# Performance work log

Measured on AMD Instinct MI355X. Metric: run time of the kernel, lower is better.

The kernel has to match this reference:

```python
import jax, jax.numpy as jnp
import numpy as np

B, S = 8, 2048
CHANNELS, DIM, HEADS = 256, 3, 6
TCH = CHANNELS * 2  # 512
EPS = 1e-5


def _linear_init(key, out_f, in_f):
    # torch nn.Linear default init: U(-1/sqrt(in_f), 1/sqrt(in_f)) for W and b
    k1, k2 = jax.random.split(key)
    bound = 1.0 / np.sqrt(in_f)
    w = jax.random.uniform(k1, (out_f, in_f), jnp.float32, -bound, bound)
    b = jax.random.uniform(k2, (out_f,), jnp.float32, -bound, bound)
    return w, b


def setup_inputs() -> dict:
    key = jax.random.key(0)
    ks = jax.random.split(key, 8)
    x = jax.random.normal(ks[0], (B, S, TCH), jnp.float32)
    wq, bq = _linear_init(ks[1], DIM, TCH)
    wk, bk = _linear_init(ks[2], DIM, TCH)
    wv, bv = _linear_init(ks[3], DIM, TCH)
    wo, bo = _linear_init(ks[4], TCH, HEADS * DIM)
    w1, b1 = _linear_init(ks[5], TCH, TCH)
    w2, b2 = _linear_init(ks[6], TCH, TCH)
    gamma = jnp.ones((TCH,), jnp.float32)
    beta = jnp.zeros((TCH,), jnp.float32)
    return {"x": x, "wq": wq, "bq": bq, "wk": wk, "bk": bk, "wv": wv, "bv": bv,
            "wo": wo, "bo": bo, "w1": w1, "b1": b1, "w2": w2, "b2": b2,
            "gamma": gamma, "beta": beta}


def _layernorm(x, gamma, beta):
    mu = jnp.mean(x, axis=-1, keepdims=True)
    var = jnp.mean(jnp.square(x - mu), axis=-1, keepdims=True)
    return (x - mu) * jax.lax.rsqrt(var + EPS) * gamma + beta


def reference(x, wq, bq, wk, bk, wv, bv, wo, bo, w1, b1, w2, b2, gamma, beta):
    # All heads share the same w_q/w_k/w_v, so one attention pass suffices;
    # concatenating HEADS copies reproduces the original math exactly.
    q = x @ wq.T + bq                      # [B,S,DIM]
    k = x @ wk.T + bk                      # [B,S,DIM]
    v = x @ wv.T + bv                      # [B,S,DIM]
    scores = jnp.einsum('bqd,bkd->bqk', q, k) / np.sqrt(DIM)  # [B,S,S]
    soft = jax.nn.softmax(scores, axis=-1)
    z = jnp.einsum('bqk,bkd->bqd', soft, v)  # [B,S,DIM]
    z = jnp.concatenate([z] * HEADS, axis=-1)  # [B,S,HEADS*DIM]
    z = z @ wo.T + bo                       # [B,S,TCH]
    r0 = x + (z @ w1.T + b1)
    r1 = _layernorm(r0, gamma, beta)
    r1 = r1 @ w2.T + b2
    r = r0 + r1
    return _layernorm(r, gamma, beta)
```

## Files before the change

kernel.cpp:

```cpp
#include <hip/hip_runtime.h>
#include <hip/hip_bf16.h>

#define TCH 512
#define MTOT 16384
#define SEQ 2048
#define LN_EPS 1e-5f

typedef __attribute__((ext_vector_type(8))) __bf16 bf16x8;
typedef __attribute__((ext_vector_type(4))) float f32x4;

__device__ __forceinline__ unsigned pkbf(float a, float b) {
  union { __hip_bfloat16 h; unsigned short u; } ca, cb;
  ca.h = __float2bfloat16(a); cb.h = __float2bfloat16(b);
  return (unsigned)ca.u | ((unsigned)cb.u << 16);
}
__device__ __forceinline__ float bf_lo(unsigned u) { return __uint_as_float(u << 16); }
__device__ __forceinline__ float bf_hi(unsigned u) { return __uint_as_float(u & 0xffff0000u); }

__device__ __forceinline__ bf16x8 cvt8(float4 a, float4 b) {
  union { __hip_bfloat16 h; __bf16 v; } u;
  bf16x8 r;
  u.h = __float2bfloat16(a.x); r[0] = u.v;
  u.h = __float2bfloat16(a.y); r[1] = u.v;
  u.h = __float2bfloat16(a.z); r[2] = u.v;
  u.h = __float2bfloat16(a.w); r[3] = u.v;
  u.h = __float2bfloat16(b.x); r[4] = u.v;
  u.h = __float2bfloat16(b.y); r[5] = u.v;
  u.h = __float2bfloat16(b.z); r[6] = u.v;
  u.h = __float2bfloat16(b.w); r[7] = u.v;
  return r;
}

#define QSCALE 0.8329517853860118f

__global__ __launch_bounds__(256) void prep_kernel(
    const float* __restrict__ w1, const float* __restrict__ w2,
    const float* __restrict__ wo, const float* __restrict__ bo,
    const float* __restrict__ wq, const float* __restrict__ bq,
    const float* __restrict__ wk, const float* __restrict__ bk,
    const float* __restrict__ wv, const float* __restrict__ bv,
    __hip_bfloat16* __restrict__ w1b, __hip_bfloat16* __restrict__ w2b,
    float4* __restrict__ wo_eff4,
    __hip_bfloat16* __restrict__ wqkvb, float* __restrict__ qkvbias)
{
  int i = blockIdx.x * 256 + threadIdx.x;
  w1b[i] = __float2bfloat16(w1[i]);
  w2b[i] = __float2bfloat16(w2[i]);
  if (i < TCH) {
    float s0 = 0.f, s1 = 0.f, s2 = 0.f;
    #pragma unroll
    for (int h = 0; h < 6; ++h) {
      s0 += wo[i*18 + h*3 + 0];
      s1 += wo[i*18 + h*3 + 1];
      s2 += wo[i*18 + h*3 + 2];
    }
    wo_eff4[i] = make_float4(s0, s1, s2, bo[i]);
  }
  if (i < 16 * TCH) {
    int row = i >> 9, k = i & 511;
    float v;
    if      (row < 3) v = wq[row * TCH + k] * QSCALE;
    else if (row < 6) v = wk[(row - 3) * TCH + k];
    else if (row < 9) v = wv[(row - 6) * TCH + k];
    else              v = 0.f;
    wqkvb[i] = __float2bfloat16(v);
  }
  if (i < 16) {
    float v;
    if      (i < 3) v = bq[i] * QSCALE;
    else if (i < 6) v = bk[i - 3];
    else if (i < 9) v = bv[i - 6];
    else            v = 0.f;
    qkvbias[i] = v;
  }
}

__global__ __launch_bounds__(256) void qkv_kernel(
    const float* __restrict__ x,
    const __hip_bfloat16* __restrict__ wqkvb, const float* __restrict__ qkvbias,
    float4* __restrict__ q4, uint4* __restrict__ kvp,
    __hip_bfloat16* __restrict__ xb)
{
  const int t = threadIdx.x, wv = t >> 6, ln = t & 63;
  const int l16 = ln & 15, quad = ln >> 4;
  const int row0 = blockIdx.x * 64 + wv * 16;

  bf16x8 bfr[16];
  #pragma unroll
  for (int ks = 0; ks < 16; ++ks)
    bfr[ks] = *reinterpret_cast<const bf16x8*>(wqkvb + l16 * TCH + ks * 32 + quad * 8);

  const float* xp = x + (size_t)(row0 + l16) * TCH + quad * 8;
  __hip_bfloat16* xo = xb + (size_t)(row0 + l16) * TCH + quad * 8;

  float4 xa0 = *(const float4*)xp,        xb0 = *(const float4*)(xp + 4);
  float4 xa1 = *(const float4*)(xp + 32), xb1 = *(const float4*)(xp + 36);
  f32x4 acc = {};
  #pragma unroll
  for (int ks = 0; ks < 16; ++ks) {
    float4 xa2 = {}, xb2 = {};
    if (ks < 14) {
      xa2 = *(const float4*)(xp + (ks + 2) * 32);
      xb2 = *(const float4*)(xp + (ks + 2) * 32 + 4);
    }
    bf16x8 af = cvt8(xa0, xb0);
    *reinterpret_cast<bf16x8*>(xo + ks * 32) = af;
    acc = __builtin_amdgcn_mfma_f32_16x16x32_bf16(af, bfr[ks], acc, 0, 0, 0);
    xa0 = xa1; xb0 = xb1; xa1 = xa2; xb1 = xb2;
  }

  __shared__ float tr[4][16][17];
  #pragma unroll
  for (int r = 0; r < 4; ++r) tr[wv][quad * 4 + r][l16] = acc[r];
  __syncthreads();

  if (ln < 32) {
    const int row  = ln & 15;
    const int grow = row0 + row;
    float c[9];
    #pragma unroll
    for (int j = 0; j < 9; ++j) c[j] = tr[wv][row][j] + qkvbias[j];
    if (ln < 16) {
      q4[grow] = make_float4(c[0], c[1], c[2], 0.f);
    } else {
      kvp[grow] = make_uint4(pkbf(c[3], c[4]), pkbf(c[5], c[6]), pkbf(c[7], c[8]), 0u);
    }
  }
}

__global__ __launch_bounds__(1024) void attn_kernel(
    const float4* __restrict__ q4, const uint4* __restrict__ kvp,
    const float4* __restrict__ wo_eff4,
    __hip_bfloat16* __restrict__ z2b)
{
  __shared__ float4 part[16 * 64];
  __shared__ float4 zbuf[64];
  __shared__ float4 woL[TCH];

  const int b    = blockIdx.x >> 5;
  const int qc   = blockIdx.x & 31;
  const int base = b * SEQ;
  const int tid  = threadIdx.x;
  for (int i = tid; i < TCH; i += 1024) woL[i] = wo_eff4[i];

  const int wave = tid >> 6;
  const int lane = tid & 63;
  const float4 q = q4[base + qc * 64 + lane];

  const int wu = __builtin_amdgcn_readfirstlane(wave);
  const uint4* kvw = kvp + base + wu * 128;

  float l[4] = {}, a0[4] = {}, a1[4] = {}, a2[4] = {};
  #pragma unroll 4
  for (int i = 0; i < 32; ++i) {
    #pragma unroll
    for (int s = 0; s < 4; ++s) {
      uint4 rec = kvw[s * 32 + i];
      float sc = bf_lo(rec.x) * q.x + bf_hi(rec.x) * q.y + bf_lo(rec.y) * q.z;
      float p = __builtin_amdgcn_exp2f(sc);
      l[s]  += p;
      a0[s] += p * bf_hi(rec.y);
      a1[s] += p * bf_lo(rec.z);
      a2[s] += p * bf_hi(rec.z);
    }
  }
  part[wave * 64 + lane] = make_float4(l[0]+l[1]+l[2]+l[3],
                                       a0[0]+a0[1]+a0[2]+a0[3],
                                       a1[0]+a1[1]+a1[2]+a1[3],
                                       a2[0]+a2[1]+a2[2]+a2[3]);
  __syncthreads();

  if (tid < 64) {
    float L = 0.f, A0 = 0.f, A1 = 0.f, A2 = 0.f;
    #pragma unroll
    for (int w = 0; w < 16; ++w) {
      float4 p = part[w * 64 + tid];
      L += p.x; A0 += p.y; A1 += p.z; A2 += p.w;
    }
    const float inv = 1.f / L;
    zbuf[tid] = make_float4(A0 * inv, A1 * inv, A2 * inv, 0.f);
  }
  __syncthreads();

  #pragma unroll
  for (int qi = 0; qi < 4; ++qi) {
    const int qloc = wave * 4 + qi;
    const float4 z = zbuf[qloc];
    unsigned* outr = (unsigned*)(z2b + (size_t)(base + qc * 64 + qloc) * TCH);
    #pragma unroll
    for (int it = 0; it < 4; ++it) {
      const int c = it * 128 + lane * 2;
      const float4 w0 = woL[c], w1 = woL[c + 1];
      outr[c >> 1] = pkbf(z.x*w0.x + z.y*w0.y + z.z*w0.z + w0.w,
                          z.x*w1.x + z.y*w1.y + z.z*w1.z + w1.w);
    }
  }
}

__global__ __launch_bounds__(256) void gemm_kernel(
    const __hip_bfloat16* __restrict__ A,
    const __hip_bfloat16* __restrict__ W,
    const float* __restrict__ bias,
    const __hip_bfloat16* __restrict__ res,
    __hip_bfloat16* __restrict__ Cout,
    float2* __restrict__ partial)
{
  __shared__ __align__(16) __hip_bfloat16 At[2][4][128][8];
  __shared__ __align__(16) __hip_bfloat16 Wt[2][4][128][8];
  __shared__ float redS[128][2];
  __shared__ float redQ[128][2];

  const int bx   = blockIdx.x;
  const int rb   = bx & 127, cb = bx >> 7;
  const int row0 = rb * 128, col0 = cb * 128;
  const int t    = threadIdx.x;
  const int w    = t >> 6, l = t & 63;
  const int l16  = l & 15, quad = l >> 4;
  const int wr   = w >> 1, wc = w & 1;
  const int srow = t & 127;
  const int sq0  = (t >> 7) << 1;

  auto stage = [&](int ks, int b) {
    #pragma unroll
    for (int j = 0; j < 2; ++j) {
      const int q = sq0 | j;
      __builtin_amdgcn_global_load_lds(
          (const __attribute__((address_space(1))) void*)(A + (size_t)(row0 + srow) * TCH + ks * 32 + q * 8),
          (__attribute__((address_space(3))) void*)&At[b][q][srow][0], 16, 0, 0);
      __builtin_amdgcn_global_load_lds(
          (const __attribute__((address_space(1))) void*)(W + (size_t)(col0 + srow) * TCH + ks * 32 + q * 8),
          (__attribute__((address_space(3))) void*)&Wt[b][q][srow][0], 16, 0, 0);
    }
  };

  f32x4 acc[4][4] = {};
  stage(0, 0);
  for (int ks = 0; ks < 16; ++ks) {
    const int cur = ks & 1;
    __syncthreads();
    if (ks < 15) stage(ks + 1, cur ^ 1);
    bf16x8 af[4], bf[4];
    #pragma unroll
    for (int mt = 0; mt < 4; ++mt)
      af[mt] = *reinterpret_cast<const bf16x8*>(&At[cur][quad][wr * 64 + mt * 16 + l16][0]);
    #pragma unroll
    for (int nt = 0; nt < 4; ++nt)
      bf[nt] = *reinterpret_cast<const bf16x8*>(&Wt[cur][quad][wc * 64 + nt * 16 + l16][0]);
    #pragma unroll
    for (int mt = 0; mt < 4; ++mt)
      #pragma unroll
      for (int nt = 0; nt < 4; ++nt)
        acc[mt][nt] = __builtin_amdgcn_mfma_f32_16x16x32_bf16(af[mt], bf[nt], acc[mt][nt], 0, 0, 0);
  }

  #pragma unroll
  for (int mt = 0; mt < 4; ++mt) {
    #pragma unroll
    for (int r = 0; r < 4; ++r) {
      const int lrow = wr * 64 + mt * 16 + quad * 4 + r;
      const int grow = row0 + lrow;
      float s = 0.f, sq = 0.f;
      #pragma unroll
      for (int nt = 0; nt < 4; ++nt) {
        const int col = col0 + wc * 64 + nt * 16 + l16;
        float v = acc[mt][nt][r] + bias[col] + __bfloat162float(res[(size_t)grow * TCH + col]);
        Cout[(size_t)grow * TCH + col] = __float2bfloat16(v);
        s += v; sq += v * v;
      }
      #pragma unroll
      for (int off = 1; off < 16; off <<= 1) {
        s  += __shfl_xor(s,  off, 64);
        sq += __shfl_xor(sq, off, 64);
      }
      if (l16 == 0) { redS[lrow][wc] = s; redQ[lrow][wc] = sq; }
    }
  }
  __syncthreads();

  if (t < 128) {
    partial[(size_t)cb * MTOT + row0 + t] =
        make_float2(redS[t][0] + redS[t][1], redQ[t][0] + redQ[t][1]);
  }
}

template<typename OUT_T>
__global__ __launch_bounds__(256) void ln_kernel(
    const __hip_bfloat16* __restrict__ Cin, const float2* __restrict__ partial,
    const float* __restrict__ gamma, const float* __restrict__ beta,
    OUT_T* __restrict__ out)
{
  const int t = threadIdx.x, wv = t >> 6, ln = t & 63;
  const int row = blockIdx.x * 4 + wv;

  float2 p0 = partial[row];
  float2 p1 = partial[MTOT + row];
  float2 p2 = partial[2 * MTOT + row];
  float2 p3 = partial[3 * MTOT + row];
  const float S = p0.x + p1.x + p2.x + p3.x;
  const float Q = p0.y + p1.y + p2.y + p3.y;
  const float mu  = S * (1.f / TCH);
  const float var = Q * (1.f / TCH) - mu * mu;
  const float rs  = rsqrtf(var + LN_EPS);

  const int c0 = ln * 8;
  bf16x8 vr = *reinterpret_cast<const bf16x8*>(Cin + (size_t)row * TCH + c0);
  float4 g0 = *(const float4*)(gamma + c0), g1 = *(const float4*)(gamma + c0 + 4);
  float4 b0 = *(const float4*)(beta  + c0), b1 = *(const float4*)(beta  + c0 + 4);

  float o[8];
  const float gg[8] = {g0.x,g0.y,g0.z,g0.w,g1.x,g1.y,g1.z,g1.w};
  const float bb[8] = {b0.x,b0.y,b0.z,b0.w,b1.x,b1.y,b1.z,b1.w};
  #pragma unroll
  for (int j = 0; j < 8; ++j) {
    union { __bf16 v; __hip_bfloat16 h; } u; u.v = vr[j];
    o[j] = (__bfloat162float(u.h) - mu) * rs * gg[j] + bb[j];
  }

  if constexpr (sizeof(OUT_T) == 2) {
    unsigned ov[4];
    #pragma unroll
    for (int j = 0; j < 4; ++j) ov[j] = pkbf(o[2*j], o[2*j+1]);
    *(uint4*)((__hip_bfloat16*)out + (size_t)row * TCH + c0) =
        make_uint4(ov[0], ov[1], ov[2], ov[3]);
  } else {
    float* op = (float*)out + (size_t)row * TCH + c0;
    *(float4*)op       = make_float4(o[0], o[1], o[2], o[3]);
    *(float4*)(op + 4) = make_float4(o[4], o[5], o[6], o[7]);
  }
}

extern "C" void kernel_launch(void* const* d_in, const int* in_sizes, int n_in,
                              void* d_out, int out_size, void* d_ws, size_t ws_size,
                              hipStream_t stream) {
  (void)in_sizes; (void)n_in; (void)out_size; (void)ws_size;
  const float* x     = (const float*)d_in[0];
  const float* wq    = (const float*)d_in[1];
  const float* bq    = (const float*)d_in[2];
  const float* wk    = (const float*)d_in[3];
  const float* bk    = (const float*)d_in[4];
  const float* wv    = (const float*)d_in[5];
  const float* bv    = (const float*)d_in[6];
  const float* wo    = (const float*)d_in[7];
  const float* bo    = (const float*)d_in[8];
  const float* w1    = (const float*)d_in[9];
  const float* b1    = (const float*)d_in[10];
  const float* w2    = (const float*)d_in[11];
  const float* b2    = (const float*)d_in[12];
  const float* gamma = (const float*)d_in[13];
  const float* beta  = (const float*)d_in[14];
  float* out = (float*)d_out;

  char* ws = (char*)d_ws;
  size_t off = 0;
  float4* q4      = (float4*)(ws + off); off += (size_t)MTOT * 16;
  uint4*  kvp     = (uint4*)(ws + off);  off += (size_t)MTOT * 16;
  float4* wo_eff4 = (float4*)(ws + off); off += (size_t)TCH * 16;
  __hip_bfloat16* w1b   = (__hip_bfloat16*)(ws + off); off += (size_t)TCH * TCH * 2;
  __hip_bfloat16* w2b   = (__hip_bfloat16*)(ws + off); off += (size_t)TCH * TCH * 2;
  __hip_bfloat16* wqkvb = (__hip_bfloat16*)(ws + off); off += (size_t)16 * TCH * 2;
  float*          qkvbias = (float*)(ws + off);        off += 64;
  __hip_bfloat16* xbb = (__hip_bfloat16*)(ws + off); off += (size_t)MTOT * TCH * 2;
  __hip_bfloat16* z2b = (__hip_bfloat16*)(ws + off); off += (size_t)MTOT * TCH * 2;
  __hip_bfloat16* r0b = (__hip_bfloat16*)(ws + off); off += (size_t)MTOT * TCH * 2;
  __hip_bfloat16* r1b = (__hip_bfloat16*)(ws + off); off += (size_t)MTOT * TCH * 2;
  __hip_bfloat16* rrb = (__hip_bfloat16*)(ws + off); off += (size_t)MTOT * TCH * 2;
  float2* part1 = (float2*)(ws + off); off += (size_t)4 * MTOT * 8;
  float2* part2 = (float2*)(ws + off); off += (size_t)4 * MTOT * 8;

  prep_kernel<<<(TCH*TCH)/256, 256, 0, stream>>>(
      w1, w2, wo, bo, wq, bq, wk, bk, wv, bv, w1b, w2b, wo_eff4, wqkvb, qkvbias);
  qkv_kernel<<<MTOT/64, 256, 0, stream>>>(x, wqkvb, qkvbias, q4, kvp, xbb);
  attn_kernel<<<MTOT/64, 1024, 0, stream>>>(q4, kvp, wo_eff4, z2b);
  gemm_kernel<<<512, 256, 0, stream>>>(z2b, w1b, b1, xbb, r0b, part1);
  ln_kernel<__hip_bfloat16><<<MTOT/4, 256, 0, stream>>>(r0b, part1, gamma, beta, r1b);
  gemm_kernel<<<512, 256, 0, stream>>>(r1b, w2b, b2, r0b, rrb, part2);
  ln_kernel<float><<<MTOT/4, 256, 0, stream>>>(rrb, part2, gamma, beta, out);
}
```

Measured before the change: 220.8 us.

## Restructure GEMM to keep full weight slice in LDS and split QKV over K

```diff
diff --git a/kernel.cpp b/kernel.cpp
--- a/kernel.cpp
+++ b/kernel.cpp
@@ -5,6 +5,8 @@
 #define MTOT 16384
 #define SEQ 2048
 #define LN_EPS 1e-5f
+#define AS1 __attribute__((address_space(1)))
+#define AS3 __attribute__((address_space(3)))
 
 typedef __attribute__((ext_vector_type(8))) __bf16 bf16x8;
 typedef __attribute__((ext_vector_type(4))) float f32x4;
@@ -81,50 +83,53 @@
     float4* __restrict__ q4, uint4* __restrict__ kvp,
     __hip_bfloat16* __restrict__ xb)
 {
-  const int t = threadIdx.x, wv = t >> 6, ln = t & 63;
+  const int t = threadIdx.x, w = t >> 6, ln = t & 63;
   const int l16 = ln & 15, quad = ln >> 4;
-  const int row0 = blockIdx.x * 64 + wv * 16;
-
-  bf16x8 bfr[16];
-  #pragma unroll
-  for (int ks = 0; ks < 16; ++ks)
-    bfr[ks] = *reinterpret_cast<const bf16x8*>(wqkvb + l16 * TCH + ks * 32 + quad * 8);
-
-  const float* xp = x + (size_t)(row0 + l16) * TCH + quad * 8;
-  __hip_bfloat16* xo = xb + (size_t)(row0 + l16) * TCH + quad * 8;
-
-  float4 xa0 = *(const float4*)xp,        xb0 = *(const float4*)(xp + 4);
-  float4 xa1 = *(const float4*)(xp + 32), xb1 = *(const float4*)(xp + 36);
+  const int row0 = blockIdx.x * 16;
+  const int kbase = w * 128 + quad * 8;
+
+  bf16x8 bfr[4];
+  #pragma unroll
+  for (int j = 0; j < 4; ++j)
+    bfr[j] = *reinterpret_cast<const bf16x8*>(wqkvb + l16 * TCH + kbase + j * 32);
+
+  const float* xp = x + (size_t)(row0 + l16) * TCH + kbase;
+  __hip_bfloat16* xo = xb + (size_t)(row0 + l16) * TCH + kbase;
+
+  float4 xa[4], xv[4];
+  #pragma unroll
+  for (int j = 0; j < 4; ++j) {
+    xa[j] = *(const float4*)(xp + j * 32);
+    xv[j] = *(const float4*)(xp + j * 32 + 4);
+  }
   f32x4 acc = {};
   #pragma unroll
-  for (int ks = 0; ks < 16; ++ks) {
-    float4 xa2 = {}, xb2 = {};
-    if (ks < 14) {
-      xa2 = *(const float4*)(xp + (ks + 2) * 32);
-      xb2 = *(const float4*)(xp + (ks + 2) * 32 + 4);
-    }
-    bf16x8 af = cvt8(xa0, xb0);
-    *reinterpret_cast<bf16x8*>(xo + ks * 32) = af;
-    acc = __builtin_amdgcn_mfma_f32_16x16x32_bf16(af, bfr[ks], acc, 0, 0, 0);
-    xa0 = xa1; xb0 = xb1; xa1 = xa2; xb1 = xb2;
-  }
-
-  __shared__ float tr[4][16][17];
-  #pragma unroll
-  for (int r = 0; r < 4; ++r) tr[wv][quad * 4 + r][l16] = acc[r];
-  __syncthreads();
-
-  if (ln < 32) {
-    const int row  = ln & 15;
-    const int grow = row0 + row;
-    float c[9];
-    #pragma unroll
-    for (int j = 0; j < 9; ++j) c[j] = tr[wv][row][j] + qkvbias[j];
-    if (ln < 16) {
-      q4[grow] = make_float4(c[0], c[1], c[2], 0.f);
-    } else {
-      kvp[grow] = make_uint4(pkbf(c[3], c[4]), pkbf(c[5], c[6]), pkbf(c[7], c[8]), 0u);
-    }
+  for (int j = 0; j < 4; ++j) {
+    bf16x8 af = cvt8(xa[j], xv[j]);
+    *reinterpret_cast<bf16x8*>(xo + j * 32) = af;
+    acc = __builtin_amdgcn_mfma_f32_16x16x32_bf16(af, bfr[j], acc, 0, 0, 0);
+  }
+
+  __shared__ float part[4][16][16];
+  __shared__ float tmp[16][17];
+  #pragma unroll
+  for (int r = 0; r < 4; ++r) part[w][quad * 4 + r][l16] = acc[r];
+  __syncthreads();
+
+  {
+    const int m = t >> 4, n = t & 15;
+    tmp[m][n] = part[0][m][n] + part[1][m][n] + part[2][m][n] + part[3][m][n]
+              + qkvbias[n];
+  }
+  __syncthreads();
+
+  if (t < 16) {
+    q4[row0 + t] = make_float4(tmp[t][0], tmp[t][1], tmp[t][2], 0.f);
+  } else if (t < 32) {
+    const int m = t - 16;
+    kvp[row0 + m] = make_uint4(pkbf(tmp[m][3], tmp[m][4]),
+                               pkbf(tmp[m][5], tmp[m][6]),
+                               pkbf(tmp[m][7], tmp[m][8]), 0u);
   }
 }
 
@@ -205,81 +210,81 @@
     __hip_bfloat16* __restrict__ Cout,
     float2* __restrict__ partial)
 {
-  __shared__ __align__(16) __hip_bfloat16 At[2][4][128][8];
-  __shared__ __align__(16) __hip_bfloat16 Wt[2][4][128][8];
-  __shared__ float redS[128][2];
-  __shared__ float redQ[128][2];
-
-  const int bx   = blockIdx.x;
-  const int rb   = bx & 127, cb = bx >> 7;
-  const int row0 = rb * 128, col0 = cb * 128;
-  const int t    = threadIdx.x;
-  const int w    = t >> 6, l = t & 63;
-  const int l16  = l & 15, quad = l >> 4;
-  const int wr   = w >> 1, wc = w & 1;
-  const int srow = t & 127;
-  const int sq0  = (t >> 7) << 1;
-
-  auto stage = [&](int ks, int b) {
-    #pragma unroll
-    for (int j = 0; j < 2; ++j) {
-      const int q = sq0 | j;
-      __builtin_amdgcn_global_load_lds(
-          (const __attribute__((address_space(1))) void*)(A + (size_t)(row0 + srow) * TCH + ks * 32 + q * 8),
-          (__attribute__((address_space(3))) void*)&At[b][q][srow][0], 16, 0, 0);
-      __builtin_amdgcn_global_load_lds(
-          (const __attribute__((address_space(1))) void*)(W + (size_t)(col0 + srow) * TCH + ks * 32 + q * 8),
-          (__attribute__((address_space(3))) void*)&Wt[b][q][srow][0], 16, 0, 0);
-    }
-  };
-
-  f32x4 acc[4][4] = {};
-  stage(0, 0);
-  for (int ks = 0; ks < 16; ++ks) {
-    const int cur = ks & 1;
-    __syncthreads();
-    if (ks < 15) stage(ks + 1, cur ^ 1);
-    bf16x8 af[4], bf[4];
-    #pragma unroll
-    for (int mt = 0; mt < 4; ++mt)
-      af[mt] = *reinterpret_cast<const bf16x8*>(&At[cur][quad][wr * 64 + mt * 16 + l16][0]);
+  __shared__ __align__(16) __hip_bfloat16 Wt[16][4][64][8];
+
+  const int bx = blockIdx.x;
+  const int cg = bx >> 6, rg = bx & 63;
+  const int col0 = cg * 64, row0 = rg * 256;
+  const int t = threadIdx.x, w = t >> 6, ln = t & 63;
+  const int l16 = ln & 15, quad = ln >> 4;
+
+  #pragma unroll
+  for (int j = 0; j < 16; ++j) {
+    const int combo = w * 16 + j;
+    const int ks = combo >> 2, q = combo & 3;
+    __builtin_amdgcn_global_load_lds(
+        (const AS1 void*)(W + (size_t)(col0 + ln) * TCH + ks * 32 + q * 8),
+        (AS3 void*)&Wt[ks][q][ln][0], 16, 0, 0);
+  }
+  __syncthreads();
+
+  float bsv[4];
+  #pragma unroll
+  for (int nt = 0; nt < 4; ++nt) bsv[nt] = bias[col0 + nt * 16 + l16];
+
+  for (int p = 0; p < 2; ++p) {
+    const int r0p = row0 + w * 64 + p * 32;
+    const __hip_bfloat16* Ab = A + (size_t)(r0p + l16) * TCH + quad * 8;
+
+    f32x4 acc[2][4] = {};
+    bf16x8 af[2], afn[2], bf[4], bfn[4];
+    af[0] = *reinterpret_cast<const bf16x8*>(Ab);
+    af[1] = *reinterpret_cast<const bf16x8*>(Ab + (size_t)16 * TCH);
     #pragma unroll
     for (int nt = 0; nt < 4; ++nt)
-      bf[nt] = *reinterpret_cast<const bf16x8*>(&Wt[cur][quad][wc * 64 + nt * 16 + l16][0]);
-    #pragma unroll
-    for (int mt = 0; mt < 4; ++mt)
-      #pragma unroll
-      for (int nt = 0; nt < 4; ++nt)
-        acc[mt][nt] = __builtin_amdgcn_mfma_f32_16x16x32_bf16(af[mt], bf[nt], acc[mt][nt], 0, 0, 0);
-  }
-
-  #pragma unroll
-  for (int mt = 0; mt < 4; ++mt) {
-    #pragma unroll
-    for (int r = 0; r < 4; ++r) {
-      const int lrow = wr * 64 + mt * 16 + quad * 4 + r;
-      const int grow = row0 + lrow;
-      float s = 0.f, sq = 0.f;
-      #pragma unroll
-      for (int nt = 0; nt < 4; ++nt) {
-        const int col = col0 + wc * 64 + nt * 16 + l16;
-        float v = acc[mt][nt][r] + bias[col] + __bfloat162float(res[(size_t)grow * TCH + col]);
-        Cout[(size_t)grow * TCH + col] = __float2bfloat16(v);
-        s += v; sq += v * v;
+      bf[nt] = *reinterpret_cast<const bf16x8*>(&Wt[0][quad][nt * 16 + l16][0]);
+
+    for (int ks = 0; ks < 16; ++ks) {
+      if (ks < 15) {
+        afn[0] = *reinterpret_cast<const bf16x8*>(Ab + (ks + 1) * 32);
+        afn[1] = *reinterpret_cast<const bf16x8*>(Ab + (size_t)16 * TCH + (ks + 1) * 32);
+        #pragma unroll
+        for (int nt = 0; nt < 4; ++nt)
+          bfn[nt] = *reinterpret_cast<const bf16x8*>(&Wt[ks + 1][quad][nt * 16 + l16][0]);
       }
       #pragma unroll
-      for (int off = 1; off < 16; off <<= 1) {
-        s  += __shfl_xor(s,  off, 64);
-        sq += __shfl_xor(sq, off, 64);
+      for (int mt = 0; mt < 2; ++mt)
+        #pragma unroll
+        for (int nt = 0; nt < 4; ++nt)
+          acc[mt][nt] = __builtin_amdgcn_mfma_f32_16x16x32_bf16(af[mt], bf[nt], acc[mt][nt], 0, 0, 0);
+      #pragma unroll
+      for (int mt = 0; mt < 2; ++mt) af[mt] = afn[mt];
+      #pragma unroll
+      for (int nt = 0; nt < 4; ++nt) bf[nt] = bfn[nt];
+    }
+
+    #pragma unroll
+    for (int mt = 0; mt < 2; ++mt) {
+      #pragma unroll
+      for (int r = 0; r < 4; ++r) {
+        const int grow = r0p + mt * 16 + quad * 4 + r;
+        float s = 0.f, sq = 0.f;
+        #pragma unroll
+        for (int nt = 0; nt < 4; ++nt) {
+          const int col = col0 + nt * 16 + l16;
+          float v = acc[mt][nt][r] + bsv[nt]
+                  + __bfloat162float(res[(size_t)grow * TCH + col]);
+          Cout[(size_t)grow * TCH + col] = __float2bfloat16(v);
+          s += v; sq += v * v;
+        }
+        #pragma unroll
+        for (int off = 1; off < 16; off <<= 1) {
+          s  += __shfl_xor(s,  off, 64);
+          sq += __shfl_xor(sq, off, 64);
+        }
+        if (l16 == 0) partial[(size_t)cg * MTOT + grow] = make_float2(s, sq);
       }
-      if (l16 == 0) { redS[lrow][wc] = s; redQ[lrow][wc] = sq; }
-    }
-  }
-  __syncthreads();
-
-  if (t < 128) {
-    partial[(size_t)cb * MTOT + row0 + t] =
-        make_float2(redS[t][0] + redS[t][1], redQ[t][0] + redQ[t][1]);
+    }
   }
 }
 
@@ -292,12 +297,12 @@
   const int t = threadIdx.x, wv = t >> 6, ln = t & 63;
   const int row = blockIdx.x * 4 + wv;
 
-  float2 p0 = partial[row];
-  float2 p1 = partial[MTOT + row];
-  float2 p2 = partial[2 * MTOT + row];
-  float2 p3 = partial[3 * MTOT + row];
-  const float S = p0.x + p1.x + p2.x + p3.x;
-  const float Q = p0.y + p1.y + p2.y + p3.y;
+  float S = 0.f, Q = 0.f;
+  #pragma unroll
+  for (int j = 0; j < 8; ++j) {
+    float2 p = partial[(size_t)j * MTOT + row];
+    S += p.x; Q += p.y;
+  }
   const float mu  = S * (1.f / TCH);
   const float var = Q * (1.f / TCH) - mu * mu;
   const float rs  = rsqrtf(var + LN_EPS);
@@ -364,12 +369,12 @@
   __hip_bfloat16* r0b = (__hip_bfloat16*)(ws + off); off += (size_t)MTOT * TCH * 2;
   __hip_bfloat16* r1b = (__hip_bfloat16*)(ws + off); off += (size_t)MTOT * TCH * 2;
   __hip_bfloat16* rrb = (__hip_bfloat16*)(ws + off); off += (size_t)MTOT * TCH * 2;
-  float2* part1 = (float2*)(ws + off); off += (size_t)4 * MTOT * 8;
-  float2* part2 = (float2*)(ws + off); off += (size_t)4 * MTOT * 8;
+  float2* part1 = (float2*)(ws + off); off += (size_t)8 * MTOT * 8;
+  float2* part2 = (float2*)(ws + off); off += (size_t)8 * MTOT * 8;
 
   prep_kernel<<<(TCH*TCH)/256, 256, 0, stream>>>(
       w1, w2, wo, bo, wq, bq, wk, bk, wv, bv, w1b, w2b, wo_eff4, wqkvb, qkvbias);
-  qkv_kernel<<<MTOT/64, 256, 0, stream>>>(x, wqkvb, qkvbias, q4, kvp, xbb);
+  qkv_kernel<<<MTOT/16, 256, 0, stream>>>(x, wqkvb, qkvbias, q4, kvp, xbb);
   attn_kernel<<<MTOT/64, 1024, 0, stream>>>(q4, kvp, wo_eff4, z2b);
   gemm_kernel<<<512, 256, 0, stream>>>(z2b, w1b, b1, xbb, r0b, part1);
   ln_kernel<__hip_bfloat16><<<MTOT/4, 256, 0, stream>>>(r0b, part1, gamma, beta, r1b);
```

New measurement: 266.9 us. +20.9%, slower.

## Fuse LayerNorm into GEMM epilogue via per-row-group ticket counter

Applied to the files above, without the earlier changes.

```diff
diff --git a/kernel.cpp b/kernel.cpp
--- a/kernel.cpp
+++ b/kernel.cpp
@@ -5,6 +5,8 @@
 #define MTOT 16384
 #define SEQ 2048
 #define LN_EPS 1e-5f
+#define AS1 __attribute__((address_space(1)))
+#define AS3 __attribute__((address_space(3)))
 
 typedef __attribute__((ext_vector_type(8))) __bf16 bf16x8;
 typedef __attribute__((ext_vector_type(4))) float f32x4;
@@ -41,11 +43,13 @@
     const float* __restrict__ wv, const float* __restrict__ bv,
     __hip_bfloat16* __restrict__ w1b, __hip_bfloat16* __restrict__ w2b,
     float4* __restrict__ wo_eff4,
-    __hip_bfloat16* __restrict__ wqkvb, float* __restrict__ qkvbias)
+    __hip_bfloat16* __restrict__ wqkvb, float* __restrict__ qkvbias,
+    unsigned* __restrict__ tickets)
 {
   int i = blockIdx.x * 256 + threadIdx.x;
   w1b[i] = __float2bfloat16(w1[i]);
   w2b[i] = __float2bfloat16(w2[i]);
+  if (i < 512) tickets[i] = 0u;
   if (i < TCH) {
     float s0 = 0.f, s1 = 0.f, s2 = 0.f;
     #pragma unroll
@@ -197,73 +201,74 @@
   }
 }
 
-__global__ __launch_bounds__(256) void gemm_kernel(
+template<typename LN_T>
+__global__ __launch_bounds__(256, 4) void gemm_ln_kernel(
     const __hip_bfloat16* __restrict__ A,
     const __hip_bfloat16* __restrict__ W,
     const float* __restrict__ bias,
     const __hip_bfloat16* __restrict__ res,
     __hip_bfloat16* __restrict__ Cout,
-    float2* __restrict__ partial)
+    float2* __restrict__ partial,
+    unsigned* __restrict__ tickets,
+    const float* __restrict__ gamma, const float* __restrict__ beta,
+    LN_T* __restrict__ LNout)
 {
-  __shared__ __align__(16) __hip_bfloat16 At[2][4][128][8];
+  __shared__ __align__(16) __hip_bfloat16 At[2][4][64][8];
   __shared__ __align__(16) __hip_bfloat16 Wt[2][4][128][8];
-  __shared__ float redS[128][2];
-  __shared__ float redQ[128][2];
-
-  const int bx   = blockIdx.x;
-  const int rb   = bx & 127, cb = bx >> 7;
-  const int row0 = rb * 128, col0 = cb * 128;
-  const int t    = threadIdx.x;
-  const int w    = t >> 6, l = t & 63;
-  const int l16  = l & 15, quad = l >> 4;
-  const int wr   = w >> 1, wc = w & 1;
-  const int srow = t & 127;
-  const int sq0  = (t >> 7) << 1;
+  __shared__ unsigned tkt;
+
+  const int bx = blockIdx.x;
+  const int rg = bx & 255, cg = bx >> 8;
+  const int row0 = rg * 64, col0 = cg * 128;
+  const int t = threadIdx.x, w = t >> 6, ln = t & 63;
+  const int l16 = ln & 15, quad = ln >> 4;
+  const int wr = w >> 1, wc = w & 1;
 
   auto stage = [&](int ks, int b) {
+    __builtin_amdgcn_global_load_lds(
+        (const AS1 void*)(A + (size_t)(row0 + ln) * TCH + ks * 32 + w * 8),
+        (AS3 void*)&At[b][w][ln][0], 16, 0, 0);
     #pragma unroll
     for (int j = 0; j < 2; ++j) {
-      const int q = sq0 | j;
+      const int q = ((t >> 7) << 1) | j;
+      const int row = t & 127;
       __builtin_amdgcn_global_load_lds(
-          (const __attribute__((address_space(1))) void*)(A + (size_t)(row0 + srow) * TCH + ks * 32 + q * 8),
-          (__attribute__((address_space(3))) void*)&At[b][q][srow][0], 16, 0, 0);
-      __builtin_amdgcn_global_load_lds(
-          (const __attribute__((address_space(1))) void*)(W + (size_t)(col0 + srow) * TCH + ks * 32 + q * 8),
-          (__attribute__((address_space(3))) void*)&Wt[b][q][srow][0], 16, 0, 0);
+          (const AS1 void*)(W + (size_t)(col0 + row) * TCH + ks * 32 + q * 8),
+          (AS3 void*)&Wt[b][q][row][0], 16, 0, 0);
     }
   };
 
-  f32x4 acc[4][4] = {};
+  f32x4 acc[2][4] = {};
   stage(0, 0);
   for (int ks = 0; ks < 16; ++ks) {
     const int cur = ks & 1;
     __syncthreads();
     if (ks < 15) stage(ks + 1, cur ^ 1);
-    bf16x8 af[4], bf[4];
-    #pragma unroll
-    for (int mt = 0; mt < 4; ++mt)
-      af[mt] = *reinterpret_cast<const bf16x8*>(&At[cur][quad][wr * 64 + mt * 16 + l16][0]);
+    bf16x8 af[2], bf[4];
+    #pragma unroll
+    for (int mt = 0; mt < 2; ++mt)
+      af[mt] = *reinterpret_cast<const bf16x8*>(&At[cur][quad][wr * 32 + mt * 16 + l16][0]);
     #pragma unroll
     for (int nt = 0; nt < 4; ++nt)
       bf[nt] = *reinterpret_cast<const bf16x8*>(&Wt[cur][quad][wc * 64 + nt * 16 + l16][0]);
     #pragma unroll
-    for (int mt = 0; mt < 4; ++mt)
+    for (int mt = 0; mt < 2; ++mt)
       #pragma unroll
       for (int nt = 0; nt < 4; ++nt)
         acc[mt][nt] = __builtin_amdgcn_mfma_f32_16x16x32_bf16(af[mt], bf[nt], acc[mt][nt], 0, 0, 0);
   }
 
   #pragma unroll
-  for (int mt = 0; mt < 4; ++mt) {
+  for (int mt = 0; mt < 2; ++mt) {
     #pragma unroll
     for (int r = 0; r < 4; ++r) {
-      const int lrow = wr * 64 + mt * 16 + quad * 4 + r;
-      const int grow = row0 + lrow;
+      const int grow = row0 + wr * 32 + mt * 16 + quad * 4 + r;
       float s = 0.f, sq = 0.f;
       #pragma unroll
       for (int nt = 0; nt < 4; ++nt) {
         const int col = col0 + wc * 64 + nt * 16 + l16;
-        float v = acc[mt][nt][r] + bias[col] + __bfloat162float(res[(size_t)grow * TCH + col]);
+        float v = acc[mt][nt][r] + bias[col]
+                + __bfloat162float(res[(size_t)grow * TCH + col]);
         Cout[(size_t)grow * TCH + col] = __float2bfloat16(v);
         s += v; sq += v * v;
       }
@@ -272,60 +277,55 @@
         s  += __shfl_xor(s,  off, 64);
         sq += __shfl_xor(sq, off, 64);
       }
-      if (l16 == 0) { redS[lrow][wc] = s; redQ[lrow][wc] = sq; }
-    }
-  }
-  __syncthreads();
-
-  if (t < 128) {
-    partial[(size_t)cb * MTOT + row0 + t] =
-        make_float2(redS[t][0] + redS[t][1], redQ[t][0] + redQ[t][1]);
-  }
-}
-
-template<typename OUT_T>
-__global__ __launch_bounds__(256) void ln_kernel(
-    const __hip_bfloat16* __restrict__ Cin, const float2* __restrict__ partial,
-    const float* __restrict__ gamma, const float* __restrict__ beta,
-    OUT_T* __restrict__ out)
-{
-  const int t = threadIdx.x, wv = t >> 6, ln = t & 63;
-  const int row = blockIdx.x * 4 + wv;
-
-  float2 p0 = partial[row];
-  float2 p1 = partial[MTOT + row];
-  float2 p2 = partial[2 * MTOT + row];
-  float2 p3 = partial[3 * MTOT + row];
-  const float S = p0.x + p1.x + p2.x + p3.x;
-  const float Q = p0.y + p1.y + p2.y + p3.y;
-  const float mu  = S * (1.f / TCH);
-  const float var = Q * (1.f / TCH) - mu * mu;
-  const float rs  = rsqrtf(var + LN_EPS);
-
-  const int c0 = ln * 8;
-  bf16x8 vr = *reinterpret_cast<const bf16x8*>(Cin + (size_t)row * TCH + c0);
-  float4 g0 = *(const float4*)(gamma + c0), g1 = *(const float4*)(gamma + c0 + 4);
-  float4 b0 = *(const float4*)(beta  + c0), b1 = *(const float4*)(beta  + c0 + 4);
-
-  float o[8];
+      if (l16 == 0)
+        partial[(size_t)(cg * 2 + wc) * MTOT + grow] = make_float2(s, sq);
+    }
+  }
+
+  __threadfence();
+  __syncthreads();
+  if (t == 0) tkt = atomicAdd(&tickets[rg], 1u);
+  __syncthreads();
+  if (tkt != 3u) return;
+  __threadfence();
+
+  const float4 g0 = *(const float4*)(gamma + ln * 8);
+  const float4 g1 = *(const float4*)(gamma + ln * 8 + 4);
+  const float4 b0 = *(const float4*)(beta + ln * 8);
+  const float4 b1 = *(const float4*)(beta + ln * 8 + 4);
   const float gg[8] = {g0.x,g0.y,g0.z,g0.w,g1.x,g1.y,g1.z,g1.w};
   const float bb[8] = {b0.x,b0.y,b0.z,b0.w,b1.x,b1.y,b1.z,b1.w};
-  #pragma unroll
-  for (int j = 0; j < 8; ++j) {
-    union { __bf16 v; __hip_bfloat16 h; } u; u.v = vr[j];
-    o[j] = (__bfloat162float(u.h) - mu) * rs * gg[j] + bb[j];
-  }
-
-  if constexpr (sizeof(OUT_T) == 2) {
-    unsigned ov[4];
-    #pragma unroll
-    for (int j = 0; j < 4; ++j) ov[j] = pkbf(o[2*j], o[2*j+1]);
-    *(uint4*)((__hip_bfloat16*)out + (size_t)row * TCH + c0) =
-        make_uint4(ov[0], ov[1], ov[2], ov[3]);
-  } else {
-    float* op = (float*)out + (size_t)row * TCH + c0;
-    *(float4*)op       = make_float4(o[0], o[1], o[2], o[3]);
-    *(float4*)(op + 4) = make_float4(o[4], o[5], o[6], o[7]);
+
+  for (int i = 0; i < 16; ++i) {
+    const int row = row0 + w * 16 + i;
+    float S = 0.f, Q = 0.f;
+    #pragma unroll
+    for (int j = 0; j < 8; ++j) {
+      float2 p = partial[(size_t)j * MTOT + row];
+      S += p.x; Q += p.y;
+    }
+    const float mu  = S * (1.f / TCH);
+    const float var = Q * (1.f / TCH) - mu * mu;
+    const float rs  = rsqrtf(var + LN_EPS);
+
+    bf16x8 vr = *reinterpret_cast<const bf16x8*>(Cout + (size_t)row * TCH + ln * 8);
+    float o[8];
+    #pragma unroll
+    for (int j = 0; j < 8; ++j) {
+      union { __bf16 v; __hip_bfloat16 h; } u; u.v = vr[j];
+      o[j] = (__bfloat162float(u.h) - mu) * rs * gg[j] + bb[j];
+    }
+    if constexpr (sizeof(LN_T) == 2) {
+      unsigned ov[4];
+      #pragma unroll
+      for (int j = 0; j < 4; ++j) ov[j] = pkbf(o[2*j], o[2*j+1]);
+      *(uint4*)((__hip_bfloat16*)LNout + (size_t)row * TCH + ln * 8) =
+          make_uint4(ov[0], ov[1], ov[2], ov[3]);
+    } else {
+      float* op = (float*)LNout + (size_t)row * TCH + ln * 8;
+      *(float4*)op       = make_float4(o[0], o[1], o[2], o[3]);
+      *(float4*)(op + 4) = make_float4(o[4], o[5], o[6], o[7]);
+    }
   }
 }
 
@@ -359,20 +359,22 @@
   __hip_bfloat16* w2b   = (__hip_bfloat16*)(ws + off); off += (size_t)TCH * TCH * 2;
   __hip_bfloat16* wqkvb = (__hip_bfloat16*)(ws + off); off += (size_t)16 * TCH * 2;
   float*          qkvbias = (float*)(ws + off);        off += 64;
+  unsigned*       tickets = (unsigned*)(ws + off);     off += 512 * 4;
   __hip_bfloat16* xbb = (__hip_bfloat16*)(ws + off); off += (size_t)MTOT * TCH * 2;
   __hip_bfloat16* z2b = (__hip_bfloat16*)(ws + off); off += (size_t)MTOT * TCH * 2;
   __hip_bfloat16* r0b = (__hip_bfloat16*)(ws + off); off += (size_t)MTOT * TCH * 2;
   __hip_bfloat16* r1b = (__hip_bfloat16*)(ws + off); off += (size_t)MTOT * TCH * 2;
   __hip_bfloat16* rrb = (__hip_bfloat16*)(ws + off); off += (size_t)MTOT * TCH * 2;
-  float2* part1 = (float2*)(ws + off); off += (size_t)4 * MTOT * 8;
-  float2* part2 = (float2*)(ws + off); off += (size_t)4 * MTOT * 8;
+  float2* part1 = (float2*)(ws + off); off += (size_t)8 * MTOT * 8;
+  float2* part2 = (float2*)(ws + off); off += (size_t)8 * MTOT * 8;
 
   prep_kernel<<<(TCH*TCH)/256, 256, 0, stream>>>(
-      w1, w2, wo, bo, wq, bq, wk, bk, wv, bv, w1b, w2b, wo_eff4, wqkvb, qkvbias);
+      w1, w2, wo, bo, wq, bq, wk, bk, wv, bv, w1b, w2b, wo_eff4, wqkvb, qkvbias,
+      tickets);
   qkv_kernel<<<MTOT/64, 256, 0, stream>>>(x, wqkvb, qkvbias, q4, kvp, xbb);
   attn_kernel<<<MTOT/64, 1024, 0, stream>>>(q4, kvp, wo_eff4, z2b);
-  gemm_kernel<<<512, 256, 0, stream>>>(z2b, w1b, b1, xbb, r0b, part1);
-  ln_kernel<__hip_bfloat16><<<MTOT/4, 256, 0, stream>>>(r0b, part1, gamma, beta, r1b);
-  gemm_kernel<<<512, 256, 0, stream>>>(r1b, w2b, b2, r0b, rrb, part2);
-  ln_kernel<float><<<MTOT/4, 256, 0, stream>>>(rrb, part2, gamma, beta, out);
-}
+  gemm_ln_kernel<__hip_bfloat16><<<1024, 256, 0, stream>>>(
+      z2b, w1b, b1, xbb, r0b, part1, tickets, gamma, beta, r1b);
+  gemm_ln_kernel<float><<<1024, 256, 0, stream>>>(
+      r1b, w2b, b2, r0b, rrb, part2, tickets + 256, gamma, beta, out);
+}
```

New measurement: 520.7 us. 2.36x slower.

## Shrink GEMM tile to 128x64, load A fragments directly to registers

Applied to the files above, without the earlier changes.

```diff
diff --git a/kernel.cpp b/kernel.cpp
--- a/kernel.cpp
+++ b/kernel.cpp
@@ -5,6 +5,8 @@
 #define MTOT 16384
 #define SEQ 2048
 #define LN_EPS 1e-5f
+#define AS1 __attribute__((address_space(1)))
+#define AS3 __attribute__((address_space(3)))
 
 typedef __attribute__((ext_vector_type(8))) __bf16 bf16x8;
 typedef __attribute__((ext_vector_type(4))) float f32x4;
@@ -205,65 +207,59 @@
     __hip_bfloat16* __restrict__ Cout,
     float2* __restrict__ partial)
 {
-  __shared__ __align__(16) __hip_bfloat16 At[2][4][128][8];
-  __shared__ __align__(16) __hip_bfloat16 Wt[2][4][128][8];
-  __shared__ float redS[128][2];
-  __shared__ float redQ[128][2];
-
-  const int bx   = blockIdx.x;
-  const int rb   = bx & 127, cb = bx >> 7;
-  const int row0 = rb * 128, col0 = cb * 128;
-  const int t    = threadIdx.x;
-  const int w    = t >> 6, l = t & 63;
-  const int l16  = l & 15, quad = l >> 4;
-  const int wr   = w >> 1, wc = w & 1;
-  const int srow = t & 127;
-  const int sq0  = (t >> 7) << 1;
+  __shared__ __align__(16) __hip_bfloat16 Wt[2][4][64][8];
+
+  const int bx = blockIdx.x;
+  const int rg = bx & 127, cg = bx >> 7;
+  const int row0 = rg * 128, col0 = cg * 64;
+  const int t = threadIdx.x, w = t >> 6, ln = t & 63;
+  const int l16 = ln & 15, quad = ln >> 4;
 
   auto stage = [&](int ks, int b) {
-    #pragma unroll
-    for (int j = 0; j < 2; ++j) {
-      const int q = sq0 | j;
-      __builtin_amdgcn_global_load_lds(
-          (const __attribute__((address_space(1))) void*)(A + (size_t)(row0 + srow) * TCH + ks * 32 + q * 8),
-          (__attribute__((address_space(3))) void*)&At[b][q][srow][0], 16, 0, 0);
-      __builtin_amdgcn_global_load_lds(
-          (const __attribute__((address_space(1))) void*)(W + (size_t)(col0 + srow) * TCH + ks * 32 + q * 8),
-          (__attribute__((address_space(3))) void*)&Wt[b][q][srow][0], 16, 0, 0);
-    }
+    __builtin_amdgcn_global_load_lds(
+        (const AS1 void*)(W + (size_t)(col0 + ln) * TCH + ks * 32 + w * 8),
+        (AS3 void*)&Wt[b][w][ln][0], 16, 0, 0);
   };
 
-  f32x4 acc[4][4] = {};
+  const __hip_bfloat16* Ab = A + (size_t)(row0 + w * 32 + l16) * TCH + quad * 8;
+
+  f32x4 acc[2][4] = {};
+  bf16x8 af[2], afn[2];
+  af[0] = *reinterpret_cast<const bf16x8*>(Ab);
+  af[1] = *reinterpret_cast<const bf16x8*>(Ab + (size_t)16 * TCH);
   stage(0, 0);
+
   for (int ks = 0; ks < 16; ++ks) {
     const int cur = ks & 1;
     __syncthreads();
-    if (ks < 15) stage(ks + 1, cur ^ 1);
-    bf16x8 af[4], bf[4];
-    #pragma unroll
-    for (int mt = 0; mt < 4; ++mt)
-      af[mt] = *reinterpret_cast<const bf16x8*>(&At[cur][quad][wr * 64 + mt * 16 + l16][0]);
+    if (ks < 15) {
+      stage(ks + 1, cur ^ 1);
+      afn[0] = *reinterpret_cast<const bf16x8*>(Ab + (ks + 1) * 32);
+      afn[1] = *reinterpret_cast<const bf16x8*>(Ab + (size_t)16 * TCH + (ks + 1) * 32);
+    }
+    bf16x8 bf[4];
     #pragma unroll
     for (int nt = 0; nt < 4; ++nt)
-      bf[nt] = *reinterpret_cast<const bf16x8*>(&Wt[cur][quad][wc * 64 + nt * 16 + l16][0]);
-    #pragma unroll
-    for (int mt = 0; mt < 4; ++mt)
+      bf[nt] = *reinterpret_cast<const bf16x8*>(&Wt[cur][quad][nt * 16 + l16][0]);
+    #pragma unroll
+    for (int mt = 0; mt < 2; ++mt)
       #pragma unroll
       for (int nt = 0; nt < 4; ++nt)
         acc[mt][nt] = __builtin_amdgcn_mfma_f32_16x16x32_bf16(af[mt], bf[nt], acc[mt][nt], 0, 0, 0);
-  }
-
-  #pragma unroll
-  for (int mt = 0; mt < 4; ++mt) {
+    af[0] = afn[0]; af[1] = afn[1];
+  }
+
+  #pragma unroll
+  for (int mt = 0; mt < 2; ++mt) {
     #pragma unroll
     for (int r = 0; r < 4; ++r) {
-      const int lrow = wr * 64 + mt * 16 + quad * 4 + r;
-      const int grow = row0 + lrow;
+      const int grow = row0 + w * 32 + mt * 16 + quad * 4 + r;
       float s = 0.f, sq = 0.f;
       #pragma unroll
       for (int nt = 0; nt < 4; ++nt) {
-        const int col = col0 + wc * 64 + nt * 16 + l16;
-        float v = acc[mt][nt][r] + bias[col] + __bfloat162float(res[(size_t)grow * TCH + col]);
+        const int col = col0 + nt * 16 + l16;
+        float v = acc[mt][nt][r] + bias[col]
+                + __bfloat162float(res[(size_t)grow * TCH + col]);
         Cout[(size_t)grow * TCH + col] = __float2bfloat16(v);
         s += v; sq += v * v;
       }
@@ -272,14 +268,8 @@
         s  += __shfl_xor(s,  off, 64);
         sq += __shfl_xor(sq, off, 64);
       }
-      if (l16 == 0) { redS[lrow][wc] = s; redQ[lrow][wc] = sq; }
-    }
-  }
-  __syncthreads();
-
-  if (t < 128) {
-    partial[(size_t)cb * MTOT + row0 + t] =
-        make_float2(redS[t][0] + redS[t][1], redQ[t][0] + redQ[t][1]);
+      if (l16 == 0) partial[(size_t)cg * MTOT + grow] = make_float2(s, sq);
+    }
   }
 }
 
@@ -292,12 +282,12 @@
   const int t = threadIdx.x, wv = t >> 6, ln = t & 63;
   const int row = blockIdx.x * 4 + wv;
 
-  float2 p0 = partial[row];
-  float2 p1 = partial[MTOT + row];
-  float2 p2 = partial[2 * MTOT + row];
-  float2 p3 = partial[3 * MTOT + row];
-  const float S = p0.x + p1.x + p2.x + p3.x;
-  const float Q = p0.y + p1.y + p2.y + p3.y;
+  float S = 0.f, Q = 0.f;
+  #pragma unroll
+  for (int j = 0; j < 8; ++j) {
+    float2 p = partial[(size_t)j * MTOT + row];
+    S += p.x; Q += p.y;
+  }
   const float mu  = S * (1.f / TCH);
   const float var = Q * (1.f / TCH) - mu * mu;
   const float rs  = rsqrtf(var + LN_EPS);
@@ -364,15 +354,15 @@
   __hip_bfloat16* r0b = (__hip_bfloat16*)(ws + off); off += (size_t)MTOT * TCH * 2;
   __hip_bfloat16* r1b = (__hip_bfloat16*)(ws + off); off += (size_t)MTOT * TCH * 2;
   __hip_bfloat16* rrb = (__hip_bfloat16*)(ws + off); off += (size_t)MTOT * TCH * 2;
-  float2* part1 = (float2*)(ws + off); off += (size_t)4 * MTOT * 8;
-  float2* part2 = (float2*)(ws + off); off += (size_t)4 * MTOT * 8;
+  float2* part1 = (float2*)(ws + off); off += (size_t)8 * MTOT * 8;
+  float2* part2 = (float2*)(ws + off); off += (size_t)8 * MTOT * 8;
 
   prep_kernel<<<(TCH*TCH)/256, 256, 0, stream>>>(
       w1, w2, wo, bo, wq, bq, wk, bk, wv, bv, w1b, w2b, wo_eff4, wqkvb, qkvbias);
   qkv_kernel<<<MTOT/64, 256, 0, stream>>>(x, wqkvb, qkvbias, q4, kvp, xbb);
   attn_kernel<<<MTOT/64, 1024, 0, stream>>>(q4, kvp, wo_eff4, z2b);
-  gemm_kernel<<<512, 256, 0, stream>>>(z2b, w1b, b1, xbb, r0b, part1);
+  gemm_kernel<<<1024, 256, 0, stream>>>(z2b, w1b, b1, xbb, r0b, part1);
   ln_kernel<__hip_bfloat16><<<MTOT/4, 256, 0, stream>>>(r0b, part1, gamma, beta, r1b);
-  gemm_kernel<<<512, 256, 0, stream>>>(r1b, w2b, b2, r0b, rrb, part2);
+  gemm_kernel<<<1024, 256, 0, stream>>>(r1b, w2b, b2, r0b, rrb, part2);
   ln_kernel<float><<<MTOT/4, 256, 0, stream>>>(rrb, part2, gamma, beta, out);
 }
```

Result: no change. 224.0 us (+1.4%).
